# Performance work log

Hardware: AMD Instinct MI355X
Metric: run time of the kernel (lower is better)

Reference implementation:

```python
import jax, jax.numpy as jnp
import numpy as np
import math

N = 100000      # num_of_nodes
E = 1600000     # edges (~avg degree 16)
F = 128         # node_feature
D = 128         # node_hidden (also topK pool size)
NR = 90000      # remaining nodes
L = 2           # num_conv_layer
LAMDA = 0.5
ALPHA = 0.1


def setup_inputs() -> dict:
    key = jax.random.key(0)
    ks = jax.random.split(key, 12)
    g = lambda k, s: jax.random.normal(k, s, jnp.float32) * 0.05
    perm = np.random.RandomState(0).permutation(N)  # disjoint remain/added split
    return {
        "x": jax.random.normal(ks[0], (N, F), jnp.float32),
        "node_scores": jax.random.normal(ks[1], (N,), jnp.float32),
        "W_hid": g(ks[2], (F, D)), "b_hid": jnp.zeros((D,), jnp.float32),
        "Wl": g(ks[3], (D, D)), "bl": jnp.zeros((D,), jnp.float32),
        "Wr": g(ks[4], (D, D)), "br": jnp.zeros((D,), jnp.float32),
        "a": g(ks[5], (1, D)),
        "h0_w": g(ks[6], (D, D)),              # initial_weight (GRU hidden init / GCN weight)
        "W_ih": g(ks[7], (3 * D, D)), "W_hh": g(ks[8], (3 * D, D)),
        "b_ih": jnp.zeros((3 * D,), jnp.float32), "b_hh": jnp.zeros((3 * D,), jnp.float32),
        "edge_index": jax.random.randint(ks[9], (2, E), 0, N),
        "remain_nodes_index": jnp.asarray(perm[:NR], jnp.int32),
        "added_nodes_index": jnp.asarray(perm[NR:], jnp.int32),
        "node_id": jnp.arange(N, dtype=jnp.int32),
    }


def _gru_step(x_in, h, W_ih, W_hh, b_ih, b_hh):
    # torch nn.GRU single step, gate order (r, z, n)
    gx = x_in @ W_ih.T + b_ih
    gh = h @ W_hh.T + b_hh
    xr, xz, xn = jnp.split(gx, 3, axis=-1)
    hr, hz, hn = jnp.split(gh, 3, axis=-1)
    r = jax.nn.sigmoid(xr + hr)
    z = jax.nn.sigmoid(xz + hz)
    n = jnp.tanh(xn + r * hn)
    return (1.0 - z) * n + z * h


def _edge_softmax_weights(edge_index, a, h_l, h_r):
    # _dynamic_self_attention_v2: per-edge scores normalized over src rows
    src, dst = edge_index[0], edge_index[1]
    al = (jax.nn.leaky_relu(h_l, 0.2) * a).sum(-1)   # [N]
    ar = (jax.nn.leaky_relu(h_r, 0.2) * a).sum(-1)   # [N]
    e = al[src] + ar[dst]                            # [E]
    e = jnp.exp(e - e.max())
    rowsum = jax.ops.segment_sum(e, src, num_segments=h_l.shape[0])
    return e / (rowsum[src] + 1e-16)


def _spmm_adj_t(edge_index, w, feats):
    # (A_trans @ feats)[i] = sum over edges with dst==i of w_e * feats[src]
    src, dst = edge_index[0], edge_index[1]
    return jax.ops.segment_sum(w[:, None] * feats[src], dst, num_segments=feats.shape[0])


def reference(x, node_scores, W_hid, b_hid, Wl, bl, Wr, br, a, h0_w, W_ih, W_hh, b_ih, b_hh, edge_index, remain_nodes_index, added_nodes_index, node_id):
    h = jax.nn.relu(x @ W_hid + b_hid)                 # [N, D]
    remain_nodes = node_id[remain_nodes_index]
    remain_x = h[remain_nodes_index]
    added_nodes = node_id[added_nodes_index]
    added_x = h[added_nodes_index]
    scores = node_scores[remain_nodes_index]
    X_res = jnp.zeros((N, D), h.dtype)
    X_res = X_res.at[remain_nodes].set(remain_x).at[added_nodes].set(added_x)
    # topK pooling branch (N > D and NR > D statically)
    _, topk = jax.lax.top_k(scores, D)
    X_pool = remain_x[topk]                            # [D, D]: GRU batch=D, feat=D
    pooling_node = remain_nodes[topk]
    h_new = _gru_step(X_pool, h0_w, W_ih, W_hh, b_ih, b_hh)  # [D, D]
    # torch: X_GCN = X_residual (alias) then in-place scatter -> both updated
    X_res = X_res.at[pooling_node].set(h_new)
    X_gcn = X_res
    Wl_X = jax.nn.relu(X_gcn @ Wl + bl)
    Wr_X = jax.nn.relu(X_gcn @ Wr + br)
    w_edge = _edge_softmax_weights(edge_index, a, Wl_X, Wr_X)
    out = X_gcn
    for l in range(1, L + 1):
        theta = math.log(LAMDA / l + 1.0)
        hi = _spmm_adj_t(edge_index, w_edge, out)
        support = (1.0 - ALPHA) * hi + ALPHA * X_res
        out = jax.nn.relu(theta * (support @ h_new) + (1.0 - theta) * support)
    return out
```

## Files before the change

kernel.cpp:

```cpp
#include <hip/hip_runtime.h>

typedef unsigned int u32;
typedef unsigned short u16;
typedef unsigned long long u64;

#define DD 128
#define ELLW 64
#define NB 196
#define BSH 9
#define BCAP 12288

typedef __attribute__((ext_vector_type(8))) short short8;
typedef __attribute__((ext_vector_type(4))) float f32x4;
union fragu { uint4 q; short8 s; };

__device__ __forceinline__ u32 mono32(float f) {
    u32 u = __float_as_uint(f);
    return (u & 0x80000000u) ? ~u : (u | 0x80000000u);
}
__device__ __forceinline__ u16 f2bf(float f) {
    u32 u = __float_as_uint(f);
    u32 r = (u + 0x7FFFu + ((u >> 16) & 1u)) >> 16;
    return (u16)r;
}
__device__ __forceinline__ float bflo(u32 p) { return __uint_as_float(p << 16); }
__device__ __forceinline__ float bfhi(u32 p) { return __uint_as_float(p & 0xFFFF0000u); }
__device__ __forceinline__ u32 packbf(float a, float b) {
    return (u32)f2bf(a) | ((u32)f2bf(b) << 16);
}

__device__ u32 block_incl_scan(u32 v, u32* wsum ) {
    int t = threadIdx.x, lane = t & 63, wid = t >> 6;
    u32 sc = v;
#pragma unroll
    for (int off = 1; off < 64; off <<= 1) {
        u32 n1 = __shfl_up(sc, off);
        if (lane >= off) sc += n1;
    }
    if (lane == 63) wsum[wid] = sc;
    __syncthreads();
    if (t < 16) {
        u32 wv = wsum[t];
#pragma unroll
        for (int off = 1; off < 16; off <<= 1) {
            u32 n1 = __shfl_up(wv, off, 16);
            if ((t & 15) >= off) wv += n1;
        }
        wsum[t] = wv;
    }
    __syncthreads();
    u32 r = sc + (wid ? wsum[wid - 1] : 0u);
    __syncthreads();
    return r;
}

__global__ __launch_bounds__(256) void k_hid(
    const float* __restrict__ x, const float* __restrict__ Wh, const float* __restrict__ bh,
    const float* __restrict__ Wr, const float* __restrict__ br, const float* __restrict__ av,
    u16* __restrict__ outBF, float* __restrict__ ear, int N) {
    __shared__ alignas(16) unsigned char As[64 * 256];
    __shared__ alignas(16) unsigned char Xs[64 * 256];
    __shared__ float spart[64];
    int t = threadIdx.x, lane = t & 63, wave = t >> 6;
    int R0 = blockIdx.x * 64;
    int brow = (lane >> 4) * 8;
    int bcol0 = wave * 32 + (lane & 15);
    if (t < 64) spart[t] = 0.f;
    fragu bfr[2][4];
#pragma unroll
    for (int ntl = 0; ntl < 2; ++ntl)
#pragma unroll
        for (int ks = 0; ks < 4; ++ks) {
            u16 h[8];
#pragma unroll
            for (int i = 0; i < 8; ++i)
                h[i] = f2bf(Wh[(size_t)(ks * 32 + brow + i) * 128 + bcol0 + ntl * 16]);
            bfr[ntl][ks].q = make_uint4((u32)h[0] | ((u32)h[1] << 16), (u32)h[2] | ((u32)h[3] << 16),
                                        (u32)h[4] | ((u32)h[5] << 16), (u32)h[6] | ((u32)h[7] << 16));
        }
    float bc[2], brc[2], avc[2];
#pragma unroll
    for (int ntl = 0; ntl < 2; ++ntl) {
        bc[ntl] = bh[bcol0 + ntl * 16];
        brc[ntl] = br[bcol0 + ntl * 16];
        avc[ntl] = av[bcol0 + ntl * 16];
    }
#pragma unroll
    for (int q2 = 0; q2 < 4; ++q2) {
        int c = t + q2 * 256;
        int row = c >> 4, c16 = c & 15;
        uint4 v = make_uint4(0u, 0u, 0u, 0u);
        if (R0 + row < N) {
            float4 f0 = ((const float4*)x)[(size_t)(R0 + row) * 32 + c16 * 2];
            float4 f1 = ((const float4*)x)[(size_t)(R0 + row) * 32 + c16 * 2 + 1];
            v.x = packbf(f0.x, f0.y);
            v.y = packbf(f0.z, f0.w);
            v.z = packbf(f1.x, f1.y);
            v.w = packbf(f1.z, f1.w);
        }
        *(uint4*)(As + row * 256 + ((c16 * 16) ^ ((row & 7) << 4))) = v;
    }
    __syncthreads();
    int arow = lane & 15, agrp = lane >> 4;
#pragma unroll
    for (int rs = 0; rs < 4; ++rs) {
        int rl = rs * 16 + arow;
        fragu afr[4];
#pragma unroll
        for (int ks = 0; ks < 4; ++ks)
            afr[ks].q = *(const uint4*)(As + rl * 256 + ((ks * 64 + agrp * 16) ^ ((rl & 7) << 4)));
#pragma unroll
        for (int ntl = 0; ntl < 2; ++ntl) {
            f32x4 acc = {0.f, 0.f, 0.f, 0.f};
#pragma unroll
            for (int ks = 0; ks < 4; ++ks)
                acc = __builtin_amdgcn_mfma_f32_16x16x32_bf16(afr[ks].s, bfr[ntl][ks].s, acc, 0, 0, 0);
            int colg = wave * 32 + ntl * 16 + (lane & 15);
#pragma unroll
            for (int r = 0; r < 4; ++r) {
                int rl2 = rs * 16 + agrp * 4 + r;
                int rowg = R0 + rl2;
                float v = fmaxf(acc[r] + bc[ntl], 0.f);
                u16 hb = f2bf(v);
                if (rowg < N) outBF[(size_t)rowg * 128 + colg] = hb;
                *(u16*)(Xs + rl2 * 256 + ((colg * 2) ^ ((rl2 & 7) << 4))) = hb;
            }
        }
    }
    fragu wfr[2][4];
#pragma unroll
    for (int ntl = 0; ntl < 2; ++ntl)
#pragma unroll
        for (int ks = 0; ks < 4; ++ks) {
            u16 h[8];
#pragma unroll
            for (int i = 0; i < 8; ++i)
                h[i] = f2bf(Wr[(size_t)(ks * 32 + brow + i) * 128 + bcol0 + ntl * 16]);
            wfr[ntl][ks].q = make_uint4((u32)h[0] | ((u32)h[1] << 16), (u32)h[2] | ((u32)h[3] << 16),
                                        (u32)h[4] | ((u32)h[5] << 16), (u32)h[6] | ((u32)h[7] << 16));
        }
    __syncthreads();
#pragma unroll
    for (int rs = 0; rs < 4; ++rs) {
        int rl = rs * 16 + arow;
        fragu afr[4];
#pragma unroll
        for (int ks = 0; ks < 4; ++ks)
            afr[ks].q = *(const uint4*)(Xs + rl * 256 + ((ks * 64 + agrp * 16) ^ ((rl & 7) << 4)));
        float part[4] = {0.f, 0.f, 0.f, 0.f};
#pragma unroll
        for (int ntl = 0; ntl < 2; ++ntl) {
            f32x4 acc = {0.f, 0.f, 0.f, 0.f};
#pragma unroll
            for (int ks = 0; ks < 4; ++ks)
                acc = __builtin_amdgcn_mfma_f32_16x16x32_bf16(afr[ks].s, wfr[ntl][ks].s, acc, 0, 0, 0);
#pragma unroll
            for (int r = 0; r < 4; ++r)
                part[r] += fmaxf(acc[r] + brc[ntl], 0.f) * avc[ntl];
        }
#pragma unroll
        for (int r = 0; r < 4; ++r) {
            float s = part[r];
            s += __shfl_xor(s, 1); s += __shfl_xor(s, 2);
            s += __shfl_xor(s, 4); s += __shfl_xor(s, 8);
            if ((lane & 15) == 0) atomicAdd(&spart[rs * 16 + agrp * 4 + r], s);
        }
    }
    __syncthreads();
    if (t < 64 && R0 + t < N) ear[R0 + t] = expf(spart[t]);
}

template <int MODE>
__global__ __launch_bounds__(256) void k_mfma(
    const u32* __restrict__ P, const u32* __restrict__ resid,
    const float* __restrict__ B, u16* __restrict__ outBF, float* __restrict__ outF,
    float theta, int N) {
    __shared__ alignas(16) unsigned char As[64 * 256];
    int t = threadIdx.x, lane = t & 63, wave = t >> 6;
    int R0 = blockIdx.x * 64;
    int brow = (lane >> 4) * 8;
    int bcol0 = wave * 32 + (lane & 15);
    fragu bfr[2][4];
#pragma unroll
    for (int ntl = 0; ntl < 2; ++ntl)
#pragma unroll
        for (int ks = 0; ks < 4; ++ks) {
            u16 h[8];
#pragma unroll
            for (int i = 0; i < 8; ++i)
                h[i] = f2bf(B[(size_t)(ks * 32 + brow + i) * 128 + bcol0 + ntl * 16]);
            bfr[ntl][ks].q = make_uint4((u32)h[0] | ((u32)h[1] << 16), (u32)h[2] | ((u32)h[3] << 16),
                                        (u32)h[4] | ((u32)h[5] << 16), (u32)h[6] | ((u32)h[7] << 16));
        }
#pragma unroll
    for (int q2 = 0; q2 < 4; ++q2) {
        int c = t + q2 * 256;
        int row = c >> 4, c16 = c & 15;
        uint4 v = make_uint4(0u, 0u, 0u, 0u);
        if (R0 + row < N) {
            uint4 pv = ((const uint4*)P)[(size_t)(R0 + row) * 16 + c16];
            uint4 xv = ((const uint4*)resid)[(size_t)(R0 + row) * 16 + c16];
            v.x = packbf(bflo(pv.x) + 0.1f * bflo(xv.x), bfhi(pv.x) + 0.1f * bfhi(xv.x));
            v.y = packbf(bflo(pv.y) + 0.1f * bflo(xv.y), bfhi(pv.y) + 0.1f * bfhi(xv.y));
            v.z = packbf(bflo(pv.z) + 0.1f * bflo(xv.z), bfhi(pv.z) + 0.1f * bfhi(xv.z));
            v.w = packbf(bflo(pv.w) + 0.1f * bflo(xv.w), bfhi(pv.w) + 0.1f * bfhi(xv.w));
        }
        *(uint4*)(As + row * 256 + ((c16 * 16) ^ ((row & 7) << 4))) = v;
    }
    __syncthreads();
    int arow = lane & 15, agrp = lane >> 4;
    float om = 1.f - theta;
#pragma unroll
    for (int rs = 0; rs < 4; ++rs) {
        int rl = rs * 16 + arow;
        fragu afr[4];
#pragma unroll
        for (int ks = 0; ks < 4; ++ks)
            afr[ks].q = *(const uint4*)(As + rl * 256 + ((ks * 64 + agrp * 16) ^ ((rl & 7) << 4)));
#pragma unroll
        for (int ntl = 0; ntl < 2; ++ntl) {
            f32x4 acc = {0.f, 0.f, 0.f, 0.f};
#pragma unroll
            for (int ks = 0; ks < 4; ++ks)
                acc = __builtin_amdgcn_mfma_f32_16x16x32_bf16(afr[ks].s, bfr[ntl][ks].s, acc, 0, 0, 0);
            int colg = wave * 32 + ntl * 16 + (lane & 15);
#pragma unroll
            for (int r = 0; r < 4; ++r) {
                int rowg = R0 + rs * 16 + agrp * 4 + r;
                if (rowg >= N) continue;
                int rl2 = rs * 16 + agrp * 4 + r;
                u16 rh = *(const u16*)(As + rl2 * 256 + ((colg * 2) ^ ((rl2 & 7) << 4)));
                float resv = __uint_as_float((u32)rh << 16);
                float v = fmaxf(theta * acc[r] + om * resv, 0.f);
                if (MODE == 2) outBF[(size_t)rowg * 128 + colg] = f2bf(v);
                else outF[(size_t)rowg * 128 + colg] = v;
            }
        }
    }
}

__global__ __launch_bounds__(256) void k_spmm(
    const u32* __restrict__ feat, const float* __restrict__ ear,
    const float* __restrict__ invS, const u32* __restrict__ cnt,
    const int* __restrict__ ell, u32* __restrict__ P, int N) {
    int w = (int)((blockIdx.x * (u32)blockDim.x + threadIdx.x) >> 6);
    int lane = threadIdx.x & 63;
    if (w >= N) return;
    int m = (int)min(cnt[w], (u32)ELLW);
    int sv = 0; float wv = 0.f;
    if (lane < m) { sv = ell[((size_t)w << 6) + lane]; wv = invS[sv]; }
    float a0 = 0.f, a1 = 0.f;
    int j = 0;
    for (; j + 8 <= m; j += 8) {
        u32 pv[8]; float wq[8];
#pragma unroll
        for (int q = 0; q < 8; ++q) {
            int s = __shfl(sv, j + q);
            wq[q] = __shfl(wv, j + q);
            pv[q] = feat[(size_t)s * 64 + lane];
        }
#pragma unroll
        for (int q = 0; q < 8; ++q) {
            a0 = fmaf(wq[q], bflo(pv[q]), a0);
            a1 = fmaf(wq[q], bfhi(pv[q]), a1);
        }
    }
    for (; j + 2 <= m; j += 2) {
        int s0 = __shfl(sv, j + 0), s1 = __shfl(sv, j + 1);
        float w0 = __shfl(wv, j + 0), w1 = __shfl(wv, j + 1);
        u32 p0 = feat[(size_t)s0 * 64 + lane];
        u32 p1 = feat[(size_t)s1 * 64 + lane];
        a0 = fmaf(w0, bflo(p0), fmaf(w1, bflo(p1), a0));
        a1 = fmaf(w0, bfhi(p0), fmaf(w1, bfhi(p1), a1));
    }
    if (j < m) {
        int s0 = __shfl(sv, j);
        float w0 = __shfl(wv, j);
        u32 p0 = feat[(size_t)s0 * 64 + lane];
        a0 = fmaf(w0, bflo(p0), a0);
        a1 = fmaf(w0, bfhi(p0), a1);
    }
    float sc = 0.9f * ear[w];
    P[(size_t)w * 64 + lane] = packbf(sc * a0, sc * a1);
}

__global__ __launch_bounds__(256) void k_bucket(
    const int* __restrict__ ei, u32* __restrict__ bD, u32* __restrict__ bS,
    u32* __restrict__ curD, u32* __restrict__ curS, int E, int nblocks) {
    __shared__ u32 cnt0[NB], cnt1[NB], pos0[NB], pos1[NB], base0[NB], base1[NB];
    int t = threadIdx.x;
    int chunk = (E + nblocks - 1) / nblocks;
    int e0 = blockIdx.x * chunk, e1 = min(E, e0 + chunk);
    for (int i = t; i < NB; i += 256) { cnt0[i] = 0; cnt1[i] = 0; pos0[i] = 0; pos1[i] = 0; }
    __syncthreads();
    for (int e = e0 + t; e < e1; e += 256) {
        int s = ei[e], d = ei[E + e];
        atomicAdd(&cnt0[d >> BSH], 1u);
        atomicAdd(&cnt1[s >> BSH], 1u);
    }
    __syncthreads();
    for (int i = t; i < NB; i += 256) {
        base0[i] = atomicAdd(&curD[i], cnt0[i]);
        base1[i] = atomicAdd(&curS[i], cnt1[i]);
    }
    __syncthreads();
    for (int e = e0 + t; e < e1; e += 256) {
        int s = ei[e], d = ei[E + e];
        int bd = d >> BSH, bs = s >> BSH;
        u32 pD = base0[bd] + atomicAdd(&pos0[bd], 1u);
        u32 pS = base1[bs] + atomicAdd(&pos1[bs], 1u);
        if (pD < (u32)BCAP) bD[(size_t)bd * BCAP + pD] = ((u32)(d & 511) << 17) | (u32)s;
        if (pS < (u32)BCAP) bS[(size_t)bs * BCAP + pS] = ((u32)(s & 511) << 17) | (u32)d;
    }
}

__global__ __launch_bounds__(256) void k_ellSsc(
    const u32* __restrict__ bD, const u32* __restrict__ bS,
    const u32* __restrict__ curD, const u32* __restrict__ curS,
    const float* __restrict__ ear,
    int* __restrict__ ell, u32* __restrict__ cnt, float* __restrict__ invS, int N) {
    __shared__ u32 lcnt[512];
    __shared__ float ls[512];
    int t = threadIdx.x;
    if (blockIdx.x < NB) {
        int b = blockIdx.x;
        for (int i = t; i < 512; i += 256) lcnt[i] = 0;
        __syncthreads();
        u32 beg = (u32)b * BCAP, end = beg + min(curD[b], (u32)BCAP);
        for (u32 e = beg + t; e < end; e += 256) {
            u32 p = bD[e];
            int dloc = (int)(p >> 17), s = (int)(p & 0x1FFFFu);
            u32 q = atomicAdd(&lcnt[dloc], 1u);
            if (q < (u32)ELLW) ell[(((size_t)(b << BSH) + dloc) << 6) + q] = s;
        }
        __syncthreads();
        int r0 = b << BSH;
        for (int i = t; i < 512; i += 256) {
            int row = r0 + i;
            if (row < N) cnt[row] = min(lcnt[i], (u32)ELLW);
        }
    } else {
        int b = blockIdx.x - NB;
        for (int i = t; i < 512; i += 256) ls[i] = 0.f;
        __syncthreads();
        u32 beg = (u32)b * BCAP, end = beg + min(curS[b], (u32)BCAP);
        for (u32 e = beg + t; e < end; e += 256) {
            u32 p = bS[e];
            int sloc = (int)(p >> 17), d = (int)(p & 0x1FFFFu);
            atomicAdd(&ls[sloc], ear[d]);
        }
        __syncthreads();
        int r0 = b << BSH;
        for (int i = t; i < 512; i += 256) {
            int row = r0 + i;
            if (row < N) invS[row] = 1.f / (ls[i] + 1e-30f);
        }
    }
}

__global__ void k_hist(const float* __restrict__ scores, const int* __restrict__ remain,
                       u32* __restrict__ hist, int NR) {
    int i = blockIdx.x * blockDim.x + threadIdx.x;
    if (i < NR) atomicAdd(&hist[mono32(scores[remain[i]]) >> 16], 1u);
}

__global__ void k_cutoff(const u32* __restrict__ hist, u32* __restrict__ misc, int K) {
    __shared__ u32 wsum[16];
    __shared__ u32 carry_s, found_s;
    int t = threadIdx.x;
    if (t == 0) { carry_s = 0; found_s = 0; }
    __syncthreads();
    for (int c = 0; c < 64; ++c) {
        int key = 65535 - ((c << 10) + t);
        u32 v = hist[key];
        u32 carry = carry_s;
        __syncthreads();
        u32 incl = block_incl_scan(v, wsum);
        u32 mycum = carry + incl;
        u32 myprev = mycum - v;
        if (mycum >= (u32)K && myprev < (u32)K) {
            misc[2] = (u32)key;
            misc[3] = myprev;
            found_s = 1;
        }
        if (t == 1023) carry_s = mycum;
        __syncthreads();
        if (found_s) return;
    }
}

__global__ void k_collect(const float* __restrict__ scores, const int* __restrict__ remain,
                          const u32* __restrict__ misc, int* __restrict__ cand,
                          u32* __restrict__ cand_cnt, int NR, int CMAX) {
    u32 B = misc[2];
    int i = blockIdx.x * blockDim.x + threadIdx.x;
    if (i < NR) {
        u32 b = mono32(scores[remain[i]]) >> 16;
        if (b >= B) {
            u32 p = atomicAdd(cand_cnt, 1u);
            if (p < (u32)CMAX) cand[p] = i;
        }
    }
}

__global__ void k_select(const float* __restrict__ scores, const int* __restrict__ remain,
                         const u32* __restrict__ misc, const int* __restrict__ cand,
                         int* __restrict__ pooling, int K, int CMAX) {
    __shared__ u64 keys[4096];
    int n = (int)min(misc[0], (u32)CMAX);
    int t = threadIdx.x;
    for (int c = t; c < n; c += 1024) {
        int i = cand[c];
        u32 m = mono32(scores[remain[i]]);
        keys[c] = ((u64)m << 32) | (u64)(0xFFFFFFFFu - (u32)i);
    }
    __syncthreads();
    for (int c = t; c < n; c += 1024) {
        u64 myk = keys[c];
        int rank = 0;
        for (int j = 0; j < n; ++j) rank += (keys[j] > myk) ? 1 : 0;
        if (rank < K) pooling[rank] = remain[cand[c]];
    }
}

__global__ void k_gru(u32* __restrict__ Xr_bf, const int* __restrict__ pooling,
                      const float* __restrict__ h0w, const float* __restrict__ Wih,
                      const float* __restrict__ Whh, const float* __restrict__ bih,
                      const float* __restrict__ bhh, const float* __restrict__ Wr,
                      const float* __restrict__ br, const float* __restrict__ av,
                      float* __restrict__ hnew, float* __restrict__ ear) {
    __shared__ float xrow[DD], hrow[DD], hn[DD];
    __shared__ float red[2];
    int j = blockIdx.x, t = threadIdx.x;
    int node = pooling[j];
    xrow[t] = __uint_as_float((u32)((const u16*)Xr_bf)[(size_t)node * DD + t] << 16);
    hrow[t] = h0w[j * DD + t];
    __syncthreads();
    float gx[3], gh[3];
#pragma unroll
    for (int g = 0; g < 3; ++g) {
        const float* wi = Wih + (g * DD + t) * DD;
        const float* wh = Whh + (g * DD + t) * DD;
        float ax = bih[g * DD + t];
        float ah = bhh[g * DD + t];
        for (int d = 0; d < DD; ++d) {
            ax += xrow[d] * wi[d];
            ah += hrow[d] * wh[d];
        }
        gx[g] = ax; gh[g] = ah;
    }
    float r = 1.f / (1.f + expf(-(gx[0] + gh[0])));
    float z = 1.f / (1.f + expf(-(gx[1] + gh[1])));
    float nn = tanhf(gx[2] + r * gh[2]);
    float hv = (1.f - z) * nn + z * hrow[t];
    hnew[j * DD + t] = hv;
    hn[t] = hv;
    __syncthreads();
    if (t < 64) Xr_bf[(size_t)node * 64 + t] = packbf(hn[2 * t], hn[2 * t + 1]);
    float acc = br[t];
    for (int k = 0; k < DD; ++k) acc += hn[k] * Wr[k * DD + t];
    float val = fmaxf(acc, 0.f) * av[t];
#pragma unroll
    for (int off = 32; off > 0; off >>= 1) val += __shfl_xor(val, off);
    if ((t & 63) == 0) red[t >> 6] = val;
    __syncthreads();
    if (t == 0) ear[node] = expf(red[0] + red[1]);
}

extern "C" void kernel_launch(void* const* d_in, const int* in_sizes, int n_in,
                              void* d_out, int out_size, void* d_ws, size_t ws_size,
                              hipStream_t stream) {
    const float* x    = (const float*)d_in[0];
    const float* nsc  = (const float*)d_in[1];
    const float* Wh   = (const float*)d_in[2];
    const float* bh   = (const float*)d_in[3];
    const float* Wr   = (const float*)d_in[6];
    const float* br   = (const float*)d_in[7];
    const float* av   = (const float*)d_in[8];
    const float* h0w  = (const float*)d_in[9];
    const float* Wih  = (const float*)d_in[10];
    const float* Whh  = (const float*)d_in[11];
    const float* bih  = (const float*)d_in[12];
    const float* bhh  = (const float*)d_in[13];
    const int* ei     = (const int*)d_in[14];
    const int* remain = (const int*)d_in[15];

    int N = in_sizes[1];
    int E = in_sizes[14] / 2;
    int NR = in_sizes[15];
    const int K = DD;
    const int CMAX = 4096;
    int mblocks = (N + 63) / 64;
    const int NBLK = 512;

    char* ws = (char*)d_ws;
    size_t off = 0;
    auto alloc = [&](size_t bytes) -> size_t {
        off = (off + 255) & ~(size_t)255;
        size_t o = off;
        off += bytes;
        return o;
    };
    size_t bucket_bytes = (size_t)2 * NB * BCAP * 4;
    size_t sup_bytes = (size_t)N * 64 * 4;
    size_t o_Xrbf = alloc((size_t)N * 64 * 4);
    size_t o_Abf  = alloc((size_t)N * 64 * 4);
    size_t o_sup  = alloc(bucket_bytes > sup_bytes ? bucket_bytes : sup_bytes);
    size_t o_ear  = alloc((size_t)N * 4);
    size_t o_ell  = alloc((size_t)N * ELLW * 4);
    size_t o_cand = alloc((size_t)CMAX * 4);
    size_t o_pool = alloc((size_t)K * 4);
    size_t o_hnew = alloc((size_t)DD * DD * 4);
    size_t o_invS = alloc((size_t)N * 4);
    size_t o_cnt  = alloc((size_t)N * 4);
    size_t o_cur  = alloc((size_t)2 * 256 * 4);
    size_t o_hist = alloc((size_t)65536 * 4);
    size_t o_misc = alloc((size_t)64 * 4);
    size_t zero_len = (o_misc + 64 * 4) - o_cur;
    (void)ws_size; (void)n_in; (void)out_size;

    u32*   Xrbf = (u32*)(ws + o_Xrbf);
    u32*   Abf  = (u32*)(ws + o_Abf);
    u32*   P    = (u32*)(ws + o_sup);
    u32*   bD   = (u32*)(ws + o_sup);
    u32*   bS   = (u32*)(ws + o_sup + (size_t)NB * BCAP * 4);
    float* ear  = (float*)(ws + o_ear);
    int*   ell  = (int*)(ws + o_ell);
    int*   cand = (int*)(ws + o_cand);
    int*   pool = (int*)(ws + o_pool);
    float* hnew = (float*)(ws + o_hnew);
    float* invS = (float*)(ws + o_invS);
    u32*   cnt  = (u32*)(ws + o_cnt);
    u32*   curD = (u32*)(ws + o_cur);
    u32*   curS = (u32*)(ws + o_cur + 256 * 4);
    u32*   hist = (u32*)(ws + o_hist);
    u32*   misc = (u32*)(ws + o_misc);

    const float theta1 = 0.40546510810816438f;
    const float theta2 = 0.22314355131420976f;

    hipMemsetAsync(ws + o_cur, 0, zero_len, stream);

    k_hid<<<mblocks, 256, 0, stream>>>(x, Wh, bh, Wr, br, av, (u16*)Xrbf, ear, N);
    k_hist<<<(NR + 255) / 256, 256, 0, stream>>>(nsc, remain, hist, NR);
    k_cutoff<<<1, 1024, 0, stream>>>(hist, misc, K);
    k_collect<<<(NR + 255) / 256, 256, 0, stream>>>(nsc, remain, misc, cand, misc, NR, CMAX);
    k_select<<<1, 1024, 0, stream>>>(nsc, remain, misc, cand, pool, K, CMAX);
    k_gru<<<K, DD, 0, stream>>>(Xrbf, pool, h0w, Wih, Whh, bih, bhh, Wr, br, av, hnew, ear);
    k_bucket<<<NBLK, 256, 0, stream>>>(ei, bD, bS, curD, curS, E, NBLK);
    k_ellSsc<<<2 * NB, 256, 0, stream>>>(bD, bS, curD, curS, ear, ell, cnt, invS, N);
    k_spmm<<<(N + 3) / 4, 256, 0, stream>>>(Xrbf, ear, invS, cnt, ell, P, N);
    k_mfma<2><<<mblocks, 256, 0, stream>>>(P, Xrbf, hnew, (u16*)Abf, nullptr, theta1, N);
    k_spmm<<<(N + 3) / 4, 256, 0, stream>>>(Abf, ear, invS, cnt, ell, P, N);
    k_mfma<3><<<mblocks, 256, 0, stream>>>(P, Xrbf, hnew, nullptr, (float*)d_out, theta2, N);
}
```

Measured before the change: 328.4 us.

## Replace padded ELL adjacency with bucket-local CSR and fold histogram into k_hid

The per-destination adjacency moves from a fixed-width 64-slot ELL array to a compact CSR stored within each bucket. Row offsets come from an in-block count pass followed by a scan, so k_ellSsc reads each bucket twice. This shrinks the adjacency footprint and makes the spmm index loads contiguous. The score histogram kernel is also merged into k_hid as extra blocks, removing one launch. Rows with more than 64 neighbours are still truncated to 64 in spmm, but all edges are now stored.

```diff
diff --git a/kernel.cpp b/kernel.cpp
--- a/kernel.cpp
+++ b/kernel.cpp
@@ -5,7 +5,6 @@
 typedef unsigned long long u64;
 
 #define DD 128
-#define ELLW 64
 #define NB 196
 #define BSH 9
 #define BCAP 12288
@@ -57,11 +56,19 @@
 __global__ __launch_bounds__(256) void k_hid(
     const float* __restrict__ x, const float* __restrict__ Wh, const float* __restrict__ bh,
     const float* __restrict__ Wr, const float* __restrict__ br, const float* __restrict__ av,
-    u16* __restrict__ outBF, float* __restrict__ ear, int N) {
+    u16* __restrict__ outBF, float* __restrict__ ear, int N, int mblocks,
+    const float* __restrict__ scores, const int* __restrict__ remain,
+    u32* __restrict__ hist, int NR) {
     __shared__ alignas(16) unsigned char As[64 * 256];
     __shared__ alignas(16) unsigned char Xs[64 * 256];
     __shared__ float spart[64];
-    int t = threadIdx.x, lane = t & 63, wave = t >> 6;
+    int t = threadIdx.x;
+    if (blockIdx.x >= mblocks) {
+        int i = (blockIdx.x - mblocks) * 256 + t;
+        if (i < NR) atomicAdd(&hist[mono32(scores[remain[i]]) >> 16], 1u);
+        return;
+    }
+    int lane = t & 63, wave = t >> 6;
     int R0 = blockIdx.x * 64;
     int brow = (lane >> 4) * 8;
     int bcol0 = wave * 32 + (lane & 15);
@@ -242,13 +249,15 @@
 __global__ __launch_bounds__(256) void k_spmm(
     const u32* __restrict__ feat, const float* __restrict__ ear,
     const float* __restrict__ invS, const u32* __restrict__ cnt,
-    const int* __restrict__ ell, u32* __restrict__ P, int N) {
+    const u32* __restrict__ rptr, const int* __restrict__ adj,
+    u32* __restrict__ P, int N) {
     int w = (int)((blockIdx.x * (u32)blockDim.x + threadIdx.x) >> 6);
     int lane = threadIdx.x & 63;
     if (w >= N) return;
-    int m = (int)min(cnt[w], (u32)ELLW);
+    int m = (int)min(cnt[w], 64u);
+    u32 base = rptr[w];
     int sv = 0; float wv = 0.f;
-    if (lane < m) { sv = ell[((size_t)w << 6) + lane]; wv = invS[sv]; }
+    if (lane < m) { sv = adj[base + lane]; wv = invS[sv]; }
     float a0 = 0.f, a1 = 0.f;
     int j = 0;
     for (; j + 8 <= m; j += 8) {
@@ -318,26 +327,56 @@
     const u32* __restrict__ bD, const u32* __restrict__ bS,
     const u32* __restrict__ curD, const u32* __restrict__ curS,
     const float* __restrict__ ear,
-    int* __restrict__ ell, u32* __restrict__ cnt, float* __restrict__ invS, int N) {
+    int* __restrict__ adj, u32* __restrict__ rptr, u32* __restrict__ cnt,
+    float* __restrict__ invS, int N) {
     __shared__ u32 lcnt[512];
+    __shared__ u32 loff[512];
+    __shared__ u32 wsum[4];
     __shared__ float ls[512];
-    int t = threadIdx.x;
+    int t = threadIdx.x, lane = t & 63, wid = t >> 6;
     if (blockIdx.x < NB) {
         int b = blockIdx.x;
         for (int i = t; i < 512; i += 256) lcnt[i] = 0;
         __syncthreads();
         u32 beg = (u32)b * BCAP, end = beg + min(curD[b], (u32)BCAP);
+        for (u32 e = beg + t; e < end; e += 256) {
+            atomicAdd(&lcnt[bD[e] >> 17], 1u);
+        }
+        __syncthreads();
+        u32 a0 = lcnt[2 * t], a1 = lcnt[2 * t + 1];
+        u32 pair = a0 + a1;
+        u32 sc = pair;
+#pragma unroll
+        for (int off2 = 1; off2 < 64; off2 <<= 1) {
+            u32 n1 = __shfl_up(sc, off2);
+            if (lane >= off2) sc += n1;
+        }
+        if (lane == 63) wsum[wid] = sc;
+        __syncthreads();
+        if (t < 4) {
+            u32 wv = wsum[t];
+#pragma unroll
+            for (int off2 = 1; off2 < 4; off2 <<= 1) {
+                u32 n1 = __shfl_up(wv, off2, 4);
+                if ((t & 3) >= off2) wv += n1;
+            }
+            wsum[t] = wv;
+        }
+        __syncthreads();
+        u32 incl = sc + (wid ? wsum[wid - 1] : 0u);
+        u32 excl = incl - pair;
+        loff[2 * t] = excl;
+        loff[2 * t + 1] = excl + a0;
+        int r0 = b << BSH;
+        if (r0 + 2 * t < N)     { rptr[r0 + 2 * t]     = beg + excl;      cnt[r0 + 2 * t]     = a0; }
+        if (r0 + 2 * t + 1 < N) { rptr[r0 + 2 * t + 1] = beg + excl + a0; cnt[r0 + 2 * t + 1] = a1; }
+        for (int i = t; i < 512; i += 256) lcnt[i] = 0;
+        __syncthreads();
         for (u32 e = beg + t; e < end; e += 256) {
             u32 p = bD[e];
             int dloc = (int)(p >> 17), s = (int)(p & 0x1FFFFu);
             u32 q = atomicAdd(&lcnt[dloc], 1u);
-            if (q < (u32)ELLW) ell[(((size_t)(b << BSH) + dloc) << 6) + q] = s;
-        }
-        __syncthreads();
-        int r0 = b << BSH;
-        for (int i = t; i < 512; i += 256) {
-            int row = r0 + i;
-            if (row < N) cnt[row] = min(lcnt[i], (u32)ELLW);
+            adj[beg + loff[dloc] + q] = s;
         }
     } else {
         int b = blockIdx.x - NB;
@@ -346,8 +385,7 @@
         u32 beg = (u32)b * BCAP, end = beg + min(curS[b], (u32)BCAP);
         for (u32 e = beg + t; e < end; e += 256) {
             u32 p = bS[e];
-            int sloc = (int)(p >> 17), d = (int)(p & 0x1FFFFu);
-            atomicAdd(&ls[sloc], ear[d]);
+            atomicAdd(&ls[p >> 17], ear[(int)(p & 0x1FFFFu)]);
         }
         __syncthreads();
         int r0 = b << BSH;
@@ -356,12 +394,6 @@
             if (row < N) invS[row] = 1.f / (ls[i] + 1e-30f);
         }
     }
-}
-
-__global__ void k_hist(const float* __restrict__ scores, const int* __restrict__ remain,
-                       u32* __restrict__ hist, int NR) {
-    int i = blockIdx.x * blockDim.x + threadIdx.x;
-    if (i < NR) atomicAdd(&hist[mono32(scores[remain[i]]) >> 16], 1u);
 }
 
 __global__ void k_cutoff(const u32* __restrict__ hist, u32* __restrict__ misc, int K) {
@@ -491,6 +523,7 @@
     const int K = DD;
     const int CMAX = 4096;
     int mblocks = (N + 63) / 64;
+    int hblocks = (NR + 255) / 256;
     const int NBLK = 512;
 
     char* ws = (char*)d_ws;
@@ -507,7 +540,8 @@
     size_t o_Abf  = alloc((size_t)N * 64 * 4);
     size_t o_sup  = alloc(bucket_bytes > sup_bytes ? bucket_bytes : sup_bytes);
     size_t o_ear  = alloc((size_t)N * 4);
-    size_t o_ell  = alloc((size_t)N * ELLW * 4);
+    size_t o_adj  = alloc((size_t)NB * BCAP * 4);
+    size_t o_rptr = alloc((size_t)N * 4);
     size_t o_cand = alloc((size_t)CMAX * 4);
     size_t o_pool = alloc((size_t)K * 4);
     size_t o_hnew = alloc((size_t)DD * DD * 4);
@@ -525,7 +559,8 @@
     u32*   bD   = (u32*)(ws + o_sup);
     u32*   bS   = (u32*)(ws + o_sup + (size_t)NB * BCAP * 4);
     float* ear  = (float*)(ws + o_ear);
-    int*   ell  = (int*)(ws + o_ell);
+    int*   adj  = (int*)(ws + o_adj);
+    u32*   rptr = (u32*)(ws + o_rptr);
     int*   cand = (int*)(ws + o_cand);
     int*   pool = (int*)(ws + o_pool);
     float* hnew = (float*)(ws + o_hnew);
@@ -541,16 +576,16 @@
 
     hipMemsetAsync(ws + o_cur, 0, zero_len, stream);
 
-    k_hid<<<mblocks, 256, 0, stream>>>(x, Wh, bh, Wr, br, av, (u16*)Xrbf, ear, N);
-    k_hist<<<(NR + 255) / 256, 256, 0, stream>>>(nsc, remain, hist, NR);
+    k_hid<<<mblocks + hblocks, 256, 0, stream>>>(x, Wh, bh, Wr, br, av, (u16*)Xrbf, ear,
+                                                 N, mblocks, nsc, remain, hist, NR);
     k_cutoff<<<1, 1024, 0, stream>>>(hist, misc, K);
     k_collect<<<(NR + 255) / 256, 256, 0, stream>>>(nsc, remain, misc, cand, misc, NR, CMAX);
     k_select<<<1, 1024, 0, stream>>>(nsc, remain, misc, cand, pool, K, CMAX);
     k_gru<<<K, DD, 0, stream>>>(Xrbf, pool, h0w, Wih, Whh, bih, bhh, Wr, br, av, hnew, ear);
     k_bucket<<<NBLK, 256, 0, stream>>>(ei, bD, bS, curD, curS, E, NBLK);
-    k_ellSsc<<<2 * NB, 256, 0, stream>>>(bD, bS, curD, curS, ear, ell, cnt, invS, N);
-    k_spmm<<<(N + 3) / 4, 256, 0, stream>>>(Xrbf, ear, invS, cnt, ell, P, N);
+    k_ellSsc<<<2 * NB, 256, 0, stream>>>(bD, bS, curD, curS, ear, adj, rptr, cnt, invS, N);
+    k_spmm<<<(N + 3) / 4, 256, 0, stream>>>(Xrbf, ear, invS, cnt, rptr, adj, P, N);
     k_mfma<2><<<mblocks, 256, 0, stream>>>(P, Xrbf, hnew, (u16*)Abf, nullptr, theta1, N);
-    k_spmm<<<(N + 3) / 4, 256, 0, stream>>>(Abf, ear, invS, cnt, ell, P, N);
+    k_spmm<<<(N + 3) / 4, 256, 0, stream>>>(Abf, ear, invS, cnt, rptr, adj, P, N);
     k_mfma<3><<<mblocks, 256, 0, stream>>>(P, Xrbf, hnew, nullptr, (float*)d_out, theta2, N);
 }
```

Measured after the change: 346.1 us. +5.4%, slower.
